# Kernel tuning notes

Hardware: AMD Instinct MI355X
Metric: run time of the kernel (lower is better)

The kernel has to match this reference:

```python
import jax, jax.numpy as jnp
import numpy as np

N_LAYERS = 3
HEADS = 2
HID = 64
IN_DIM = 10
NEG_SLOPE = 0.2  # DGL EGATConv leaky_relu default
B, NPG = 8, 6250  # batch_size, nodes per graph (== max_n_nodes)
N = B * NPG
E = 500000
N_RES = 30  # max_n_resources


def _mlp2(x, W0, b0, W1, b1):
    return jax.nn.relu(x @ W0 + b0) @ W1 + b1


def _segment_softmax(e, dst, n):
    # softmax over incoming edges of each destination node (DGL edge_softmax)
    m = jax.ops.segment_max(e, dst, num_segments=n)
    m = jnp.where(jnp.isfinite(m), m, 0.0)
    ex = jnp.exp(e - m[dst])
    s = jax.ops.segment_sum(ex, dst, num_segments=n)
    return ex / (s[dst] + 1e-9)


def _egat(h, f, src, dst, W_ni, W_nj, W_fij, W_node, attn, bias):
    # per-edge attention features: f_ni[src] + f_nj[dst] + f_fij + bias
    f_out = (h @ W_ni)[src] + (h @ W_nj)[dst] + f @ W_fij + bias   # (E, H*HID)
    f_out = jax.nn.leaky_relu(f_out, NEG_SLOPE).reshape(-1, HEADS, HID)
    e = (f_out * attn[None]).sum(-1)                               # (E, H)
    alpha = _segment_softmax(e, dst, h.shape[0])
    msg = alpha[:, :, None] * (h @ W_node).reshape(-1, HEADS, HID)[src]
    h_out = jax.ops.segment_sum(msg, dst, num_segments=h.shape[0])  # (N, H, HID)
    return h_out, f_out


def _forward(feat, att_rc, att_rp, etype_emb, rid_emb, rc_W, rc_b, rp_W, rp_b,
             fe_W0, fe_b0, fe_W1, fe_b1,
             W_ni, W_nj, W_fij, W_node, attn, egat_bias,
             Wm0, bm0, Wm1, bm1, src, dst, etype, rid):
    feats_list = [feat]
    h = _mlp2(feat, fe_W0, fe_b0, fe_W1, fe_b1)
    feats_list.append(h)
    # 'sum' edge embedding flavor
    emb = etype_emb[etype] + rid_emb[rid] + (att_rc @ rc_W + rc_b) + (att_rp @ rp_W + rp_b)
    for l in range(N_LAYERS):
        h_att, _ = _egat(h, emb, src, dst, W_ni[l], W_nj[l], W_fij[l], W_node[l],
                         attn[l], egat_bias[l])
        h = _mlp2(h_att.reshape(-1, HEADS * HID), Wm0[l], bm0[l], Wm1[l], bm1[l]) + feats_list[-1]
        feats_list.append(h)
    features = jnp.concatenate(feats_list, axis=1)       # (N, IN_DIM + HID*(L+1))
    node_features = features.reshape(B, NPG, -1)
    graph_embedding = node_features.max(axis=1)          # graph_pooling='max'
    rep = jnp.broadcast_to(graph_embedding[:, None, :], node_features.shape)
    return jnp.concatenate([node_features, rep], axis=2)  # (B, NPG, 2*F)


def setup_inputs():
    key = jax.random.key(0)
    ks = iter(jax.random.split(key, 40))
    def rn(shape, s=0.1):
        return jax.random.normal(next(ks), shape, dtype=jnp.float32) * s
    HO = HEADS * HID
    inp = {}
    inp['feat'] = rn((N, IN_DIM), 1.0)
    inp['att_rc'] = rn((E, 2), 1.0)
    inp['att_rp'] = rn((E, 3), 1.0)
    inp['etype_emb'] = rn((7, HID))
    inp['rid_emb'] = rn((N_RES + 1, HID))
    inp['rc_W'] = rn((2, HID)); inp['rc_b'] = rn((HID,))
    inp['rp_W'] = rn((3, HID)); inp['rp_b'] = rn((HID,))
    inp['fe_W0'] = rn((IN_DIM, HID)); inp['fe_b0'] = rn((HID,))
    inp['fe_W1'] = rn((HID, HID)); inp['fe_b1'] = rn((HID,))
    inp['W_ni'] = rn((N_LAYERS, HID, HO)); inp['W_nj'] = rn((N_LAYERS, HID, HO))
    inp['W_fij'] = rn((N_LAYERS, HID, HO)); inp['W_node'] = rn((N_LAYERS, HID, HO))
    inp['attn'] = rn((N_LAYERS, HEADS, HID)); inp['egat_bias'] = rn((N_LAYERS, HO))
    inp['Wm0'] = rn((N_LAYERS, HO, HO)); inp['bm0'] = rn((N_LAYERS, HO))
    inp['Wm1'] = rn((N_LAYERS, HO, HID)); inp['bm1'] = rn((N_LAYERS, HID))
    inp['src'] = jax.random.randint(next(ks), (E,), 0, N, dtype=jnp.int32)
    inp['dst'] = jax.random.randint(next(ks), (E,), 0, N, dtype=jnp.int32)
    inp['etype'] = jax.random.randint(next(ks), (E,), 0, 7, dtype=jnp.int32)
    inp['rid'] = jax.random.randint(next(ks), (E,), 0, N_RES + 1, dtype=jnp.int32)
    return inp


def reference(feat, att_rc, att_rp, etype_emb, rid_emb, rc_W, rc_b, rp_W, rp_b,
              fe_W0, fe_b0, fe_W1, fe_b1, W_ni, W_nj, W_fij, W_node, attn, egat_bias,
              Wm0, bm0, Wm1, bm1, src, dst, etype, rid):
    return _forward(feat, att_rc, att_rp, etype_emb, rid_emb, rc_W, rc_b, rp_W, rp_b,
                    fe_W0, fe_b0, fe_W1, fe_b1, W_ni, W_nj, W_fij, W_node, attn, egat_bias,
                    Wm0, bm0, Wm1, bm1, src, dst, etype, rid)
```

## Files before the change

kernel.cpp:

```cpp
#include <hip/hip_runtime.h>
#include <hip/hip_bf16.h>
#include <math.h>

#define N_NODES 50000
#define N_EDGES 500000
#define B_GRAPHS 8
#define NPG 6250
#define HID 64
#define HO 128
#define IN_DIM 10
#define F_TOT 266
#define OUT_C 532
#define NEG_SLOPE 0.2f
#define NT_ROWS 44
#define SCB 200
#define SCH 250

typedef short bf16x8 __attribute__((ext_vector_type(8)));
typedef float f32x4 __attribute__((ext_vector_type(4)));
typedef float f32x2 __attribute__((ext_vector_type(2)));
typedef unsigned u32x2v __attribute__((ext_vector_type(2)));

__device__ __forceinline__ float LD(const void* p, size_t i, int f32) {
    if (f32) return ((const float*)p)[i];
    unsigned u = ((const unsigned short*)p)[i];
    return __uint_as_float(u << 16);
}
__device__ __forceinline__ unsigned fkey(float f) {
    unsigned b = __float_as_uint(f);
    return (b & 0x80000000u) ? ~b : (b | 0x80000000u);
}
__device__ __forceinline__ float funkey(unsigned k) {
    unsigned b = (k & 0x80000000u) ? (k & 0x7fffffffu) : ~k;
    return __uint_as_float(b);
}
__device__ __forceinline__ unsigned short rnebf(float x) {
    unsigned u = __float_as_uint(x);
    return (unsigned short)((u + 0x7FFFu + ((u >> 16) & 1u)) >> 16);
}
__device__ __forceinline__ unsigned pk2(float lo, float hi) {
    return (unsigned)rnebf(lo) | ((unsigned)rnebf(hi) << 16);
}
__device__ __forceinline__ float plo(unsigned u) { return __uint_as_float(u << 16); }
__device__ __forceinline__ float phi(unsigned u) { return __uint_as_float(u & 0xFFFF0000u); }
__device__ __forceinline__ f32x2 up2(unsigned u) {
    return (f32x2){__uint_as_float(u << 16), __uint_as_float(u & 0xFFFF0000u)};
}
__device__ __forceinline__ void pswap(float& a, float& b) {
    u32x2v r = __builtin_amdgcn_permlane32_swap(__float_as_uint(a), __float_as_uint(b),
                                                false, false);
    a = __uint_as_float(r.x);
    b = __uint_as_float(r.y);
}

__global__ void k_detect(const void* __restrict__ att_rc, int* __restrict__ flagp) {
    __shared__ int cnt;
    if (threadIdx.x == 0) cnt = 0;
    __syncthreads();
    const unsigned short* w = (const unsigned short*)att_rc;
    int c = 0;
    for (int i = threadIdx.x; i < 8192; i += 256) {
        unsigned e = (w[i] >> 7) & 0xFF;
        if (e >= 0xC0) c++;
    }
    atomicAdd(&cnt, c);
    __syncthreads();
    if (threadIdx.x == 0) *flagp = (cnt > 8) ? 1 : 0;
}

__global__ void k_wprep(const void* __restrict__ W_ni, const void* __restrict__ W_nj,
                        const void* __restrict__ W_node, const void* __restrict__ Wm0,
                        const void* __restrict__ Wm1,
                        unsigned short* __restrict__ pw_n,
                        unsigned short* __restrict__ pw_m0,
                        unsigned short* __restrict__ pw_m1,
                        const int* __restrict__ flagp) {
    const int f32 = *flagp;
    int i = blockIdx.x * 256 + threadIdx.x;
    if (i < 73728) {
        int k = i & 63, c = (i >> 6) & 127, lm = i >> 13;
        int m = lm % 3, l = lm / 3;
        const void* W = (m == 0) ? W_ni : (m == 1) ? W_nj : W_node;
        pw_n[i] = rnebf(LD(W, (size_t)l * 8192 + k * 128 + c, f32));
    } else if (i < 73728 + 49152) {
        int j = i - 73728;
        int k = j & 127, c = (j >> 7) & 127, l = j >> 14;
        pw_m0[j] = rnebf(LD(Wm0, (size_t)l * 16384 + k * 128 + c, f32));
    } else if (i < 147456) {
        int j = i - 122880;
        int k = j & 127, c = (j >> 7) & 63, l = j >> 13;
        pw_m1[j] = rnebf(LD(Wm1, (size_t)l * 8192 + k * 64 + c, f32));
    }
}

__global__ void k_count(const int* __restrict__ dst, int* __restrict__ cnt) {
    int i = blockIdx.x * blockDim.x + threadIdx.x;
    int stride = gridDim.x * blockDim.x;
    for (int e = i; e < N_EDGES; e += stride) atomicAdd(&cnt[dst[e]], 1);
}

__global__ void k_scan1(const int* __restrict__ cnt, int* __restrict__ bsum) {
    __shared__ int red[256];
    int b = blockIdx.x, t = threadIdx.x;
    red[t] = (t < SCH) ? cnt[b * SCH + t] : 0;
    __syncthreads();
    for (int off = 128; off; off >>= 1) {
        if (t < off) red[t] += red[t + off];
        __syncthreads();
    }
    if (t == 0) bsum[b] = red[0];
}
__global__ void k_scan2(const int* __restrict__ bsum, int* __restrict__ boff) {
    __shared__ int ts[256];
    int t = threadIdx.x;
    int v = (t < SCB) ? bsum[t] : 0;
    ts[t] = v;
    __syncthreads();
    for (int off = 1; off < 256; off <<= 1) {
        int u = (t >= off) ? ts[t - off] : 0;
        __syncthreads();
        ts[t] += u;
        __syncthreads();
    }
    if (t < SCB) boff[t] = ts[t] - v;
}
__global__ void k_scan3(const int* __restrict__ cnt, const int* __restrict__ boff,
                        int* __restrict__ rowptr, int* __restrict__ cursor) {
    __shared__ int ts[256];
    int b = blockIdx.x, t = threadIdx.x;
    int base = b * SCH;
    int v = (t < SCH) ? cnt[base + t] : 0;
    ts[t] = v;
    __syncthreads();
    for (int off = 1; off < 256; off <<= 1) {
        int u = (t >= off) ? ts[t - off] : 0;
        __syncthreads();
        ts[t] += u;
        __syncthreads();
    }
    if (t < SCH) {
        int r = boff[b] + ts[t] - v;
        rowptr[base + t] = r;
        cursor[base + t] = r;
    }
    if (b == SCB - 1 && t == SCH - 1) rowptr[N_NODES] = boff[b] + ts[t];
}

__global__ void k_fill(const int* __restrict__ src, const int* __restrict__ dst,
                       const int* __restrict__ etype, const int* __restrict__ rid,
                       const void* __restrict__ att_rc, const void* __restrict__ att_rp,
                       int* __restrict__ cursor, uint4* __restrict__ emeta,
                       const int* __restrict__ flagp) {
    const int f32 = *flagp;
    int i = blockIdx.x * blockDim.x + threadIdx.x;
    int stride = gridDim.x * blockDim.x;
    for (int e = i; e < N_EDGES; e += stride) {
        int d = dst[e];
        int j = atomicAdd(&cursor[d], 1);
        float rc0 = LD(att_rc, 2 * (size_t)e, f32), rc1 = LD(att_rc, 2 * (size_t)e + 1, f32);
        float rp0 = LD(att_rp, 3 * (size_t)e, f32), rp1 = LD(att_rp, 3 * (size_t)e + 1, f32),
              rp2 = LD(att_rp, 3 * (size_t)e + 2, f32);
        uint4 m;
        m.x = pk2(rc0, rc1);
        m.y = pk2(rp0, rp1);
        m.z = pk2(rp2, 0.f);
        m.w = (unsigned)(etype[e] | (rid[e] << 3) | ((unsigned)src[e] << 8));
        emeta[j] = m;
    }
}

__global__ void k_init(const void* __restrict__ feat,
                       const void* __restrict__ W0, const void* __restrict__ b0,
                       const void* __restrict__ W1, const void* __restrict__ b1,
                       float* __restrict__ feats, const int* __restrict__ flagp) {
    const int f32 = *flagp;
    __shared__ float sf[64 * 12];
    __shared__ float sW0[IN_DIM * 64];
    __shared__ float sb0[64], sb1[64];
    __shared__ float sh[64 * 64];
    __shared__ float sW1[64 * 64];
    int tid = threadIdx.x, n0 = blockIdx.x * 64;
    for (int i = tid; i < IN_DIM * 64; i += 256) sW0[i] = LD(W0, i, f32);
    for (int i = tid; i < 64; i += 256) { sb0[i] = LD(b0, i, f32); sb1[i] = LD(b1, i, f32); }
    for (int i = tid; i < 64 * 64; i += 256) sW1[i] = LD(W1, i, f32);
    for (int i = tid; i < 64 * IN_DIM; i += 256) {
        int n = n0 + i / IN_DIM, c = i % IN_DIM;
        sf[(i / IN_DIM) * 12 + c] = (n < N_NODES) ? LD(feat, (size_t)n * IN_DIM + c, f32) : 0.f;
    }
    __syncthreads();
    int ng = tid / 16, cg = tid % 16;
    float acc[4][4];
    #pragma unroll
    for (int i = 0; i < 4; i++)
        #pragma unroll
        for (int j = 0; j < 4; j++) acc[i][j] = sb0[cg * 4 + j];
    #pragma unroll
    for (int k = 0; k < IN_DIM; k++)
        #pragma unroll
        for (int i = 0; i < 4; i++) {
            float a = sf[(ng * 4 + i) * 12 + k];
            #pragma unroll
            for (int j = 0; j < 4; j++) acc[i][j] += a * sW0[k * 64 + cg * 4 + j];
        }
    #pragma unroll
    for (int i = 0; i < 4; i++)
        #pragma unroll
        for (int j = 0; j < 4; j++) sh[(ng * 4 + i) * 64 + cg * 4 + j] = fmaxf(acc[i][j], 0.f);
    __syncthreads();
    float o[4][4];
    #pragma unroll
    for (int i = 0; i < 4; i++)
        #pragma unroll
        for (int j = 0; j < 4; j++) o[i][j] = sb1[cg * 4 + j];
    for (int k = 0; k < 64; k++) {
        float4 bv = *(const float4*)&sW1[k * 64 + cg * 4];
        #pragma unroll
        for (int i = 0; i < 4; i++) {
            float a = sh[(ng * 4 + i) * 64 + k];
            o[i][0] += a * bv.x; o[i][1] += a * bv.y;
            o[i][2] += a * bv.z; o[i][3] += a * bv.w;
        }
    }
    #pragma unroll
    for (int i = 0; i < 4; i++) {
        int n = n0 + ng * 4 + i;
        if (n < N_NODES) {
            float* r = feats + (size_t)n * F_TOT;
            #pragma unroll
            for (int j = 0; j < 4; j++) r[IN_DIM + cg * 4 + j] = o[i][j];
        }
    }
    for (int i = tid; i < 64 * IN_DIM; i += 256) {
        int n = n0 + i / IN_DIM, c = i % IN_DIM;
        if (n < N_NODES) feats[(size_t)n * F_TOT + c] = sf[(i / IN_DIM) * 12 + c];
    }
}

__global__ void k_tables(const void* __restrict__ etype_emb, const void* __restrict__ rid_emb,
                         const void* __restrict__ rc_W, const void* __restrict__ rc_b,
                         const void* __restrict__ rp_W, const void* __restrict__ rp_b,
                         const void* __restrict__ W_fij, const void* __restrict__ egat_bias,
                         float* __restrict__ T, const int* __restrict__ flagp) {
    const int f32 = *flagp;
    int l = blockIdx.x;
    __shared__ float S[NT_ROWS * HID];
    __shared__ float W[HID * HO];
    for (int i = threadIdx.x; i < 7 * HID; i += 256) S[i] = LD(etype_emb, i, f32);
    for (int i = threadIdx.x; i < 31 * HID; i += 256) S[7 * HID + i] = LD(rid_emb, i, f32);
    for (int i = threadIdx.x; i < 2 * HID; i += 256) S[38 * HID + i] = LD(rc_W, i, f32);
    for (int i = threadIdx.x; i < 3 * HID; i += 256) S[40 * HID + i] = LD(rp_W, i, f32);
    for (int i = threadIdx.x; i < HID; i += 256)
        S[43 * HID + i] = LD(rc_b, i, f32) + LD(rp_b, i, f32);
    for (int i = threadIdx.x; i < HID * HO; i += 256)
        W[i] = LD(W_fij, (size_t)l * HID * HO + i, f32);
    __syncthreads();
    for (int idx = threadIdx.x; idx < NT_ROWS * HO; idx += 256) {
        int r = idx / HO, c = idx % HO;
        float acc = (r == 43) ? LD(egat_bias, l * HO + c, f32) : 0.f;
        for (int k = 0; k < HID; k++) acc += S[r * HID + k] * W[k * HO + c];
        T[(size_t)l * NT_ROWS * HO + idx] = acc;
    }
}

__global__ void __launch_bounds__(256) k_ngemm(
        const float* __restrict__ feats, int h_off,
        const unsigned short* __restrict__ pw_n, int l,
        unsigned* __restrict__ gsrc, unsigned* __restrict__ gdst) {
    __shared__ __align__(16) unsigned short Xs[64 * 72];
    __shared__ __align__(16) unsigned short Ws[384 * 72];
    int tid = threadIdx.x, n0 = blockIdx.x * 64;
    for (int i = tid; i < 64 * 64; i += 256) {
        int n = i >> 6, c = i & 63, gn = n0 + n;
        Xs[n * 72 + c] = rnebf((gn < N_NODES) ? feats[(size_t)gn * F_TOT + h_off + c] : 0.f);
    }
    const uint4* pn = (const uint4*)pw_n + (size_t)l * 3072;
    for (int i = tid; i < 3072; i += 256) {
        int kq = i & 7, mc = i >> 3;
        *(uint4*)&Ws[mc * 72 + kq * 8] = pn[i];
    }
    __syncthreads();
    int wid = tid >> 6, lane = tid & 63;
    int row0 = wid * 16, mrow = lane & 15, quad = lane >> 4;
    bf16x8 a0 = *(const bf16x8*)&Xs[(row0 + mrow) * 72 + quad * 8];
    bf16x8 a1 = *(const bf16x8*)&Xs[(row0 + mrow) * 72 + 32 + quad * 8];
    f32x4 accA[8], accB[8];
    #pragma unroll
    for (int j = 0; j < 8; j++) { accA[j] = (f32x4){0,0,0,0}; accB[j] = (f32x4){0,0,0,0}; }
    #pragma unroll
    for (int j = 0; j < 8; j++) {
        bf16x8 b0 = *(const bf16x8*)&Ws[(0 * 128 + j * 16 + mrow) * 72 + quad * 8];
        bf16x8 b1 = *(const bf16x8*)&Ws[(0 * 128 + j * 16 + mrow) * 72 + 32 + quad * 8];
        accA[j] = __builtin_amdgcn_mfma_f32_16x16x32_bf16(a0, b0, accA[j], 0, 0, 0);
        accA[j] = __builtin_amdgcn_mfma_f32_16x16x32_bf16(a1, b1, accA[j], 0, 0, 0);
        bf16x8 c0 = *(const bf16x8*)&Ws[(2 * 128 + j * 16 + mrow) * 72 + quad * 8];
        bf16x8 c1 = *(const bf16x8*)&Ws[(2 * 128 + j * 16 + mrow) * 72 + 32 + quad * 8];
        accB[j] = __builtin_amdgcn_mfma_f32_16x16x32_bf16(a0, c0, accB[j], 0, 0, 0);
        accB[j] = __builtin_amdgcn_mfma_f32_16x16x32_bf16(a1, c1, accB[j], 0, 0, 0);
    }
    #pragma unroll
    for (int j = 0; j < 4; j++) {
        int c = j * 16 + mrow;
        #pragma unroll
        for (int r = 0; r < 4; r++) {
            int gn = n0 + row0 + quad * 4 + r;
            if (gn < N_NODES) {
                uint2 v;
                v.x = pk2(accA[j][r], accA[j + 4][r]);
                v.y = pk2(accB[j][r], accB[j + 4][r]);
                *(uint2*)&gsrc[(size_t)gn * 128 + c * 2] = v;
            }
        }
    }
    f32x4 accC[8];
    #pragma unroll
    for (int j = 0; j < 8; j++) accC[j] = (f32x4){0,0,0,0};
    #pragma unroll
    for (int j = 0; j < 8; j++) {
        bf16x8 b0 = *(const bf16x8*)&Ws[(1 * 128 + j * 16 + mrow) * 72 + quad * 8];
        bf16x8 b1 = *(const bf16x8*)&Ws[(1 * 128 + j * 16 + mrow) * 72 + 32 + quad * 8];
        accC[j] = __builtin_amdgcn_mfma_f32_16x16x32_bf16(a0, b0, accC[j], 0, 0, 0);
        accC[j] = __builtin_amdgcn_mfma_f32_16x16x32_bf16(a1, b1, accC[j], 0, 0, 0);
    }
    #pragma unroll
    for (int j = 0; j < 4; j++) {
        int c = j * 16 + mrow;
        #pragma unroll
        for (int r = 0; r < 4; r++) {
            int gn = n0 + row0 + quad * 4 + r;
            if (gn < N_NODES)
                gdst[(size_t)gn * 64 + c] = pk2(accC[j][r], accC[j + 4][r]);
        }
    }
}

__global__ void __launch_bounds__(256) k_edge_fused(
        const float* __restrict__ T, const void* __restrict__ attn, int l,
        const unsigned* __restrict__ gsrc, const unsigned* __restrict__ gdst,
        const int* __restrict__ rowptr, const uint4* __restrict__ emeta,
        float* __restrict__ h_att, const int* __restrict__ flagp) {
    const int f32 = *flagp;
    __shared__ f32x2 Ts2[38 * 64];
    const float* Tl = T + (size_t)l * NT_ROWS * HO;
    int tid = threadIdx.x;
    for (int i = tid; i < 38 * 64; i += 256) {
        int r = i >> 6, c = i & 63;
        Ts2[i] = (f32x2){Tl[r * HO + c], Tl[r * HO + 64 + c]};
    }
    int lane = tid & 63;
    f32x2 C2[6];
    #pragma unroll
    for (int r = 0; r < 6; r++)
        C2[r] = (f32x2){Tl[(38 + r) * HO + lane], Tl[(38 + r) * HO + 64 + lane]};
    const float LOG2E = 1.4426950408889634f;
    f32x2 AT2 = (f32x2){LD(attn, l * HO + lane, f32) * LOG2E,
                        LD(attn, l * HO + 64 + lane, f32) * LOG2E};
    __syncthreads();
    int wid = tid >> 6;
    int d0 = blockIdx.x * 8 + wid * 2;

    #pragma unroll 1
    for (int dn = 0; dn < 2; dn++) {
        int d = d0 + dn;
        int jb = __builtin_amdgcn_readfirstlane(rowptr[d]);
        int je = __builtin_amdgcn_readfirstlane(rowptr[d + 1]);
        int last = je - 1;
        if (last < jb) last = jb;
        if (last > N_EDGES - 1) last = N_EDGES - 1;
        unsigned gd = gdst[(size_t)d * 64 + lane];
        f32x2 NJ2 = up2(gd) + C2[5];
        f32x2 A2 = (f32x2){0.f, 0.f};
        float Lsp = 0.f;

        auto fe = [&](int j_) -> uint4 {
            int jj = (j_ < last) ? j_ : last;
            jj = __builtin_amdgcn_readfirstlane(jj);
            return emeta[jj];
        };
        auto fg = [&](const uint4& em) -> uint2 {
            return *(const uint2*)&gsrc[(size_t)(em.w >> 8) * 128 + lane * 2];
        };
        auto logits = [&](const uint4& em, const uint2& g, float& s_out, f32x2& h2) {
            int et = (int)(em.w & 7u), ri = (int)((em.w >> 3) & 31u);
            f32x2 x = up2(g.x) + NJ2;
            x += Ts2[et * 64 + lane];
            x += Ts2[(7 + ri) * 64 + lane];
            x += plo(em.x) * C2[0];
            x += phi(em.x) * C2[1];
            x += plo(em.y) * C2[2];
            x += phi(em.y) * C2[3];
            x += plo(em.z) * C2[4];
            f32x2 xs = x * NEG_SLOPE;
            x = __builtin_elementwise_max(x, xs);
            f32x2 p = x * AT2;
            h2 = up2(g.y);
            float pa = p.x, pb = p.y;
            pswap(pa, pb);
            float s = pa + pb;
            s += __int_as_float(__builtin_amdgcn_update_dpp(0, __float_as_int(s), 0xB1, 0xF, 0xF, true));
            s += __int_as_float(__builtin_amdgcn_update_dpp(0, __float_as_int(s), 0x4E, 0xF, 0xF, true));
            s += __int_as_float(__builtin_amdgcn_update_dpp(0, __float_as_int(s), 0x141, 0xF, 0xF, true));
            s += __int_as_float(__builtin_amdgcn_update_dpp(0, __float_as_int(s), 0x140, 0xF, 0xF, true));
            s += __int_as_float(__builtin_amdgcn_ds_swizzle(__float_as_int(s), 0x401F));
            s_out = s;
        };
        auto upd = [&](float w, f32x2 h2) {
            Lsp += w;
            float wa = w, wb = w;
            pswap(wa, wb);
            A2 += (f32x2){wa, wb} * h2;
        };

        uint4 eA0 = fe(jb),     eA1 = fe(jb + 1), eA2 = fe(jb + 2), eA3 = fe(jb + 3);
        uint4 eB0 = fe(jb + 4), eB1 = fe(jb + 5), eB2 = fe(jb + 6), eB3 = fe(jb + 7);
        uint2 gA0 = fg(eA0), gA1 = fg(eA1), gA2 = fg(eA2), gA3 = fg(eA3);
        int j = jb;
        #pragma unroll 1
        while (j < je) {
            uint4 eC0 = fe(j + 8), eC1 = fe(j + 9), eC2 = fe(j + 10), eC3 = fe(j + 11);
            uint2 gB0 = fg(eB0), gB1 = fg(eB1), gB2 = fg(eB2), gB3 = fg(eB3);
            {
                float s0, s1, s2, s3;
                f32x2 h0, h1, h2v, h3;
                logits(eA0, gA0, s0, h0);
                logits(eA1, gA1, s1, h1);
                logits(eA2, gA2, s2, h2v);
                logits(eA3, gA3, s3, h3);
                float w0 = __builtin_exp2f(s0);
                float w1 = (j + 1 < je) ? __builtin_exp2f(s1) : 0.f;
                float w2 = (j + 2 < je) ? __builtin_exp2f(s2) : 0.f;
                float w3 = (j + 3 < je) ? __builtin_exp2f(s3) : 0.f;
                upd(w0, h0); upd(w1, h1); upd(w2, h2v); upd(w3, h3);
            }
            if (j + 4 >= je) break;
            uint4 eD0 = fe(j + 12), eD1 = fe(j + 13), eD2 = fe(j + 14), eD3 = fe(j + 15);
            uint2 gN0 = fg(eC0), gN1 = fg(eC1), gN2 = fg(eC2), gN3 = fg(eC3);
            {
                float s0, s1, s2, s3;
                f32x2 h0, h1, h2v, h3;
                logits(eB0, gB0, s0, h0);
                logits(eB1, gB1, s1, h1);
                logits(eB2, gB2, s2, h2v);
                logits(eB3, gB3, s3, h3);
                float w0 = __builtin_exp2f(s0);
                float w1 = (j + 5 < je) ? __builtin_exp2f(s1) : 0.f;
                float w2 = (j + 6 < je) ? __builtin_exp2f(s2) : 0.f;
                float w3 = (j + 7 < je) ? __builtin_exp2f(s3) : 0.f;
                upd(w0, h0); upd(w1, h1); upd(w2, h2v); upd(w3, h3);
            }
            eA0 = eC0; eA1 = eC1; eA2 = eC2; eA3 = eC3;
            eB0 = eD0; eB1 = eD1; eB2 = eD2; eB3 = eD3;
            gA0 = gN0; gA1 = gN1; gA2 = gN2; gA3 = gN3;
            j += 8;
        }

        float la = Lsp, lb = Lsp;
        pswap(la, lb);
        h_att[(size_t)d * HO + lane]      = A2.x / (la + 1e-9f);
        h_att[(size_t)d * HO + 64 + lane] = A2.y / (lb + 1e-9f);
    }
}

__global__ void __launch_bounds__(256) k_mlp(
        const float* __restrict__ h_att,
        const unsigned short* __restrict__ pw_m0, const void* __restrict__ bm0,
        const unsigned short* __restrict__ pw_m1, const void* __restrict__ bm1, int l,
        float* __restrict__ feats, int prev_off, int out_off,
        const int* __restrict__ flagp) {
    const int f32 = *flagp;
    __shared__ __align__(16) unsigned short Xs[64 * 136];
    __shared__ __align__(16) unsigned short W0T[128 * 136];
    __shared__ __align__(16) unsigned short W1T[64 * 136];
    __shared__ float sb0[HO], sb1[64];
    int tid = threadIdx.x, n0 = blockIdx.x * 64;
    for (int i = tid; i < 64 * 128; i += 256) {
        int n = i >> 7, c = i & 127, gn = n0 + n;
        Xs[n * 136 + c] = rnebf((gn < N_NODES) ? h_att[(size_t)gn * HO + c] : 0.f);
    }
    const uint4* p0 = (const uint4*)pw_m0 + (size_t)l * 2048;
    for (int i = tid; i < 2048; i += 256) {
        int kq = i & 15, c = i >> 4;
        *(uint4*)&W0T[c * 136 + kq * 8] = p0[i];
    }
    const uint4* p1 = (const uint4*)pw_m1 + (size_t)l * 1024;
    for (int i = tid; i < 1024; i += 256) {
        int kq = i & 15, c = i >> 4;
        *(uint4*)&W1T[c * 136 + kq * 8] = p1[i];
    }
    for (int i = tid; i < HO; i += 256) sb0[i] = LD(bm0, l * HO + i, f32);
    for (int i = tid; i < 64; i += 256) sb1[i] = LD(bm1, l * 64 + i, f32);
    __syncthreads();
    int wid = tid >> 6, lane = tid & 63;
    int row0 = wid * 16, mrow = lane & 15, quad = lane >> 4;
    f32x4 acc[8];
    #pragma unroll
    for (int j = 0; j < 8; j++) {
        float b = sb0[j * 16 + mrow];
        acc[j] = (f32x4){b, b, b, b};
    }
    #pragma unroll
    for (int ks = 0; ks < 4; ks++) {
        bf16x8 a = *(const bf16x8*)&Xs[(row0 + mrow) * 136 + ks * 32 + quad * 8];
        #pragma unroll
        for (int j = 0; j < 8; j++) {
            bf16x8 b = *(const bf16x8*)&W0T[(j * 16 + mrow) * 136 + ks * 32 + quad * 8];
            acc[j] = __builtin_amdgcn_mfma_f32_16x16x32_bf16(a, b, acc[j], 0, 0, 0);
        }
    }
    #pragma unroll
    for (int j = 0; j < 8; j++)
        #pragma unroll
        for (int r = 0; r < 4; r++)
            Xs[(row0 + quad * 4 + r) * 136 + j * 16 + mrow] = rnebf(fmaxf(acc[j][r], 0.f));
    f32x4 o[4];
    #pragma unroll
    for (int j = 0; j < 4; j++) {
        float b = sb1[j * 16 + mrow];
        o[j] = (f32x4){b, b, b, b};
    }
    #pragma unroll
    for (int ks = 0; ks < 4; ks++) {
        bf16x8 a = *(const bf16x8*)&Xs[(row0 + mrow) * 136 + ks * 32 + quad * 8];
        #pragma unroll
        for (int j = 0; j < 4; j++) {
            bf16x8 b = *(const bf16x8*)&W1T[(j * 16 + mrow) * 136 + ks * 32 + quad * 8];
            o[j] = __builtin_amdgcn_mfma_f32_16x16x32_bf16(a, b, o[j], 0, 0, 0);
        }
    }
    #pragma unroll
    for (int j = 0; j < 4; j++) {
        int c = j * 16 + mrow;
        #pragma unroll
        for (int r = 0; r < 4; r++) {
            int gn = n0 + row0 + quad * 4 + r;
            if (gn < N_NODES) {
                float* rw = feats + (size_t)gn * F_TOT;
                rw[out_off + c] = o[j][r] + rw[prev_off + c];
            }
        }
    }
}

__global__ void k_pool(const float* __restrict__ feats, unsigned* __restrict__ gmax) {
    int g = blockIdx.x;
    int chunk = blockIdx.y;
    int t = threadIdx.x;
    const int CS = 49;
    int nb = chunk * CS;
    int ne = (nb + CS < NPG) ? nb + CS : NPG;
    float m0 = -INFINITY, m1 = -INFINITY;
    for (int n = nb; n < ne; n++) {
        const float* row = feats + (size_t)(g * NPG + n) * F_TOT;
        m0 = fmaxf(m0, row[t]);
        if (t + 256 < F_TOT) m1 = fmaxf(m1, row[t + 256]);
    }
    atomicMax(&gmax[g * F_TOT + t], fkey(m0));
    if (t + 256 < F_TOT) atomicMax(&gmax[g * F_TOT + t + 256], fkey(m1));
}

__global__ void k_out(const float* __restrict__ feats, const unsigned* __restrict__ gmax,
                      void* __restrict__ out, const int* __restrict__ flagp) {
    const int f32 = *flagp;
    int lane = threadIdx.x & 63;
    int wave = (blockIdx.x * blockDim.x + threadIdx.x) >> 6;
    int nw = (gridDim.x * blockDim.x) >> 6;
    for (int row = wave; row < B_GRAPHS * NPG; row += nw) {
        int g = row / NPG;
        const float* fr = feats + (size_t)row * F_TOT;
        const unsigned* gr = gmax + g * F_TOT;
        if (f32) {
            float* o = (float*)out + (size_t)row * OUT_C;
            for (int c = lane; c < OUT_C; c += 64)
                o[c] = (c < F_TOT) ? fr[c] : funkey(gr[c - F_TOT]);
        } else {
            __hip_bfloat16* o = (__hip_bfloat16*)out + (size_t)row * OUT_C;
            for (int c = lane; c < OUT_C; c += 64)
                o[c] = __float2bfloat16((c < F_TOT) ? fr[c] : funkey(gr[c - F_TOT]));
        }
    }
}

extern "C" void kernel_launch(void* const* d_in, const int* in_sizes, int n_in,
                              void* d_out, int out_size, void* d_ws, size_t ws_size,
                              hipStream_t stream) {
    const void* feat      = d_in[0];
    const void* att_rc    = d_in[1];
    const void* att_rp    = d_in[2];
    const void* etype_emb = d_in[3];
    const void* rid_emb   = d_in[4];
    const void* rc_W      = d_in[5];
    const void* rc_b      = d_in[6];
    const void* rp_W      = d_in[7];
    const void* rp_b      = d_in[8];
    const void* fe_W0     = d_in[9];
    const void* fe_b0     = d_in[10];
    const void* fe_W1     = d_in[11];
    const void* fe_b1     = d_in[12];
    const void* W_ni      = d_in[13];
    const void* W_nj      = d_in[14];
    const void* W_fij     = d_in[15];
    const void* W_node    = d_in[16];
    const void* attn      = d_in[17];
    const void* egat_bias = d_in[18];
    const void* Wm0       = d_in[19];
    const void* bm0       = d_in[20];
    const void* Wm1       = d_in[21];
    const void* bm1       = d_in[22];
    const int* src   = (const int*)d_in[23];
    const int* dst   = (const int*)d_in[24];
    const int* etype = (const int*)d_in[25];
    const int* rid   = (const int*)d_in[26];

    char* p = (char*)d_ws;
    auto alloc = [&](size_t bytes) {
        char* r = p;
        p += (bytes + 255) & ~(size_t)255;
        return r;
    };
    float*    feats  = (float*)alloc((size_t)N_NODES * F_TOT * 4);
    unsigned* gsrc   = (unsigned*)alloc((size_t)N_NODES * HO * 4);
    unsigned* gdst   = (unsigned*)alloc((size_t)N_NODES * 64 * 4);
    float*    h_att  = (float*)alloc((size_t)N_NODES * HO * 4);
    float*    T      = (float*)alloc((size_t)3 * NT_ROWS * HO * 4);
    unsigned* gmax   = (unsigned*)alloc((size_t)B_GRAPHS * F_TOT * 4);
    int*      flagp  = (int*)alloc(256);
    int*      rowptr = (int*)alloc((size_t)(N_NODES + 1) * 4);
    int*      cursor = (int*)alloc((size_t)N_NODES * 4);
    int*      cnt    = (int*)alloc((size_t)N_NODES * 4);
    int*      bsum   = (int*)alloc((size_t)SCB * 4);
    int*      boff   = (int*)alloc((size_t)SCB * 4);
    uint4*    emeta  = (uint4*)alloc((size_t)N_EDGES * 16);
    unsigned short* pw_n  = (unsigned short*)alloc((size_t)73728 * 2);
    unsigned short* pw_m0 = (unsigned short*)alloc((size_t)49152 * 2);
    unsigned short* pw_m1 = (unsigned short*)alloc((size_t)24576 * 2);

    k_detect<<<1, 256, 0, stream>>>(att_rc, flagp);
    hipMemsetAsync(cnt, 0, (size_t)N_NODES * 4, stream);
    hipMemsetAsync(gmax, 0, (size_t)B_GRAPHS * F_TOT * 4, stream);
    k_wprep<<<576, 256, 0, stream>>>(W_ni, W_nj, W_node, Wm0, Wm1,
                                     pw_n, pw_m0, pw_m1, flagp);
    k_count<<<512, 256, 0, stream>>>(dst, cnt);
    k_scan1<<<SCB, 256, 0, stream>>>(cnt, bsum);
    k_scan2<<<1, 256, 0, stream>>>(bsum, boff);
    k_scan3<<<SCB, 256, 0, stream>>>(cnt, boff, rowptr, cursor);
    k_fill<<<1024, 256, 0, stream>>>(src, dst, etype, rid, att_rc, att_rp,
                                     cursor, emeta, flagp);
    k_init<<<(N_NODES + 63) / 64, 256, 0, stream>>>(feat, fe_W0, fe_b0, fe_W1, fe_b1,
                                                    feats, flagp);
    k_tables<<<3, 256, 0, stream>>>(etype_emb, rid_emb, rc_W, rc_b, rp_W, rp_b,
                                    W_fij, egat_bias, T, flagp);
    for (int l = 0; l < 3; l++) {
        int h_off = IN_DIM + l * HID;
        int out_off = IN_DIM + (l + 1) * HID;
        k_ngemm<<<(N_NODES + 63) / 64, 256, 0, stream>>>(feats, h_off, pw_n, l, gsrc, gdst);
        k_edge_fused<<<N_NODES / 8, 256, 0, stream>>>(T, attn, l, gsrc, gdst,
                                                      rowptr, emeta, h_att, flagp);
        k_mlp<<<(N_NODES + 63) / 64, 256, 0, stream>>>(h_att, pw_m0, bm0, pw_m1, bm1, l,
                                                       feats, h_off, out_off, flagp);
    }
    k_pool<<<dim3(B_GRAPHS, 128), 256, 0, stream>>>(feats, gmax);
    k_out<<<2048, 256, 0, stream>>>(feats, gmax, d_out, flagp);
}
```

Measured before the change: 720.1 us.

## Fuse next-layer node GEMM into MLP kernel and merge setup kernels

The node projection GEMM for the next layer is folded into the MLP kernel's epilogue. The freshly computed h stays in shared memory as bf16 and feeds MFMA directly, so k_ngemm does not have to reload it from feats. Setup work is also consolidated: the memsets and k_tables go into k_wprep as extra blocks, and scan2 is merged into scan3 by having each block reduce its own prefix of the block sums. This removes several launches and a global round-trip of h, at the cost of a larger shared-memory footprint in k_mlp (about 72 KB), which can lower occupancy.

```diff
diff --git a/kernel.cpp b/kernel.cpp
--- a/kernel.cpp
+++ b/kernel.cpp
@@ -74,22 +74,59 @@
                         unsigned short* __restrict__ pw_n,
                         unsigned short* __restrict__ pw_m0,
                         unsigned short* __restrict__ pw_m1,
-                        const int* __restrict__ flagp) {
+                        const int* __restrict__ flagp,
+                        const void* __restrict__ etype_emb, const void* __restrict__ rid_emb,
+                        const void* __restrict__ rc_W, const void* __restrict__ rc_b,
+                        const void* __restrict__ rp_W, const void* __restrict__ rp_b,
+                        const void* __restrict__ W_fij, const void* __restrict__ egat_bias,
+                        float* __restrict__ T,
+                        int* __restrict__ cnt, unsigned* __restrict__ gmax) {
+    __shared__ float S[NT_ROWS * HID];
+    __shared__ float W[HID * HO];
     const int f32 = *flagp;
-    int i = blockIdx.x * 256 + threadIdx.x;
-    if (i < 73728) {
-        int k = i & 63, c = (i >> 6) & 127, lm = i >> 13;
-        int m = lm % 3, l = lm / 3;
-        const void* W = (m == 0) ? W_ni : (m == 1) ? W_nj : W_node;
-        pw_n[i] = rnebf(LD(W, (size_t)l * 8192 + k * 128 + c, f32));
-    } else if (i < 73728 + 49152) {
-        int j = i - 73728;
-        int k = j & 127, c = (j >> 7) & 127, l = j >> 14;
-        pw_m0[j] = rnebf(LD(Wm0, (size_t)l * 16384 + k * 128 + c, f32));
-    } else if (i < 147456) {
-        int j = i - 122880;
-        int k = j & 127, c = (j >> 7) & 63, l = j >> 13;
-        pw_m1[j] = rnebf(LD(Wm1, (size_t)l * 8192 + k * 64 + c, f32));
+    int b = blockIdx.x;
+    if (b < 576) {
+        int i = b * 256 + threadIdx.x;
+        if (i < 73728) {
+            int k = i & 63, c = (i >> 6) & 127, lm = i >> 13;
+            int m = lm % 3, l = lm / 3;
+            const void* Wp = (m == 0) ? W_ni : (m == 1) ? W_nj : W_node;
+            pw_n[i] = rnebf(LD(Wp, (size_t)l * 8192 + k * 128 + c, f32));
+        } else if (i < 73728 + 49152) {
+            int j = i - 73728;
+            int k = j & 127, c = (j >> 7) & 127, l = j >> 14;
+            pw_m0[j] = rnebf(LD(Wm0, (size_t)l * 16384 + k * 128 + c, f32));
+        } else if (i < 147456) {
+            int j = i - 122880;
+            int k = j & 127, c = (j >> 7) & 63, l = j >> 13;
+            pw_m1[j] = rnebf(LD(Wm1, (size_t)l * 8192 + k * 64 + c, f32));
+        }
+    } else if (b < 780) {
+        int i2 = (b - 576) * 256 + threadIdx.x;
+        if (i2 < N_NODES) cnt[i2] = 0;
+        else {
+            int g = i2 - N_NODES;
+            if (g < B_GRAPHS * F_TOT) gmax[g] = 0;
+        }
+    } else {
+        int l = b - 780;
+        if (l < 3) {
+            for (int i = threadIdx.x; i < 7 * HID; i += 256) S[i] = LD(etype_emb, i, f32);
+            for (int i = threadIdx.x; i < 31 * HID; i += 256) S[7 * HID + i] = LD(rid_emb, i, f32);
+            for (int i = threadIdx.x; i < 2 * HID; i += 256) S[38 * HID + i] = LD(rc_W, i, f32);
+            for (int i = threadIdx.x; i < 3 * HID; i += 256) S[40 * HID + i] = LD(rp_W, i, f32);
+            for (int i = threadIdx.x; i < HID; i += 256)
+                S[43 * HID + i] = LD(rc_b, i, f32) + LD(rp_b, i, f32);
+            for (int i = threadIdx.x; i < HID * HO; i += 256)
+                W[i] = LD(W_fij, (size_t)l * HID * HO + i, f32);
+            __syncthreads();
+            for (int idx = threadIdx.x; idx < NT_ROWS * HO; idx += 256) {
+                int r = idx / HO, c = idx % HO;
+                float acc = (r == 43) ? LD(egat_bias, l * HO + c, f32) : 0.f;
+                for (int k = 0; k < HID; k++) acc += S[r * HID + k] * W[k * HO + c];
+                T[(size_t)l * NT_ROWS * HO + idx] = acc;
+            }
+        }
     }
 }
 
@@ -110,10 +147,21 @@
     }
     if (t == 0) bsum[b] = red[0];
 }
-__global__ void k_scan2(const int* __restrict__ bsum, int* __restrict__ boff) {
+__global__ void k_scan3(const int* __restrict__ cnt, const int* __restrict__ bsum,
+                        int* __restrict__ rowptr, int* __restrict__ cursor) {
+    __shared__ int red[256];
     __shared__ int ts[256];
-    int t = threadIdx.x;
-    int v = (t < SCB) ? bsum[t] : 0;
+    int b = blockIdx.x, t = threadIdx.x;
+    red[t] = (t < b && t < SCB) ? bsum[t] : 0;
+    __syncthreads();
+    for (int off = 128; off; off >>= 1) {
+        if (t < off) red[t] += red[t + off];
+        __syncthreads();
+    }
+    int boff_b = red[0];
+    __syncthreads();
+    int base = b * SCH;
+    int v = (t < SCH) ? cnt[base + t] : 0;
     ts[t] = v;
     __syncthreads();
     for (int off = 1; off < 256; off <<= 1) {
@@ -122,28 +170,12 @@
         ts[t] += u;
         __syncthreads();
     }
-    if (t < SCB) boff[t] = ts[t] - v;
-}
-__global__ void k_scan3(const int* __restrict__ cnt, const int* __restrict__ boff,
-                        int* __restrict__ rowptr, int* __restrict__ cursor) {
-    __shared__ int ts[256];
-    int b = blockIdx.x, t = threadIdx.x;
-    int base = b * SCH;
-    int v = (t < SCH) ? cnt[base + t] : 0;
-    ts[t] = v;
-    __syncthreads();
-    for (int off = 1; off < 256; off <<= 1) {
-        int u = (t >= off) ? ts[t - off] : 0;
-        __syncthreads();
-        ts[t] += u;
-        __syncthreads();
-    }
     if (t < SCH) {
-        int r = boff[b] + ts[t] - v;
+        int r = boff_b + ts[t] - v;
         rowptr[base + t] = r;
         cursor[base + t] = r;
     }
-    if (b == SCB - 1 && t == SCH - 1) rowptr[N_NODES] = boff[b] + ts[t];
+    if (b == SCB - 1 && t == SCH - 1) rowptr[N_NODES] = boff_b + ts[t];
 }
 
 __global__ void k_fill(const int* __restrict__ src, const int* __restrict__ dst,
@@ -233,32 +265,6 @@
     for (int i = tid; i < 64 * IN_DIM; i += 256) {
         int n = n0 + i / IN_DIM, c = i % IN_DIM;
         if (n < N_NODES) feats[(size_t)n * F_TOT + c] = sf[(i / IN_DIM) * 12 + c];
-    }
-}
-
-__global__ void k_tables(const void* __restrict__ etype_emb, const void* __restrict__ rid_emb,
-                         const void* __restrict__ rc_W, const void* __restrict__ rc_b,
-                         const void* __restrict__ rp_W, const void* __restrict__ rp_b,
-                         const void* __restrict__ W_fij, const void* __restrict__ egat_bias,
-                         float* __restrict__ T, const int* __restrict__ flagp) {
-    const int f32 = *flagp;
-    int l = blockIdx.x;
-    __shared__ float S[NT_ROWS * HID];
-    __shared__ float W[HID * HO];
-    for (int i = threadIdx.x; i < 7 * HID; i += 256) S[i] = LD(etype_emb, i, f32);
-    for (int i = threadIdx.x; i < 31 * HID; i += 256) S[7 * HID + i] = LD(rid_emb, i, f32);
-    for (int i = threadIdx.x; i < 2 * HID; i += 256) S[38 * HID + i] = LD(rc_W, i, f32);
-    for (int i = threadIdx.x; i < 3 * HID; i += 256) S[40 * HID + i] = LD(rp_W, i, f32);
-    for (int i = threadIdx.x; i < HID; i += 256)
-        S[43 * HID + i] = LD(rc_b, i, f32) + LD(rp_b, i, f32);
-    for (int i = threadIdx.x; i < HID * HO; i += 256)
-        W[i] = LD(W_fij, (size_t)l * HID * HO + i, f32);
-    __syncthreads();
-    for (int idx = threadIdx.x; idx < NT_ROWS * HO; idx += 256) {
-        int r = idx / HO, c = idx % HO;
-        float acc = (r == 43) ? LD(egat_bias, l * HO + c, f32) : 0.f;
-        for (int k = 0; k < HID; k++) acc += S[r * HID + k] * W[k * HO + c];
-        T[(size_t)l * NT_ROWS * HO + idx] = acc;
     }
 }
 
@@ -465,12 +471,17 @@
         const unsigned short* __restrict__ pw_m0, const void* __restrict__ bm0,
         const unsigned short* __restrict__ pw_m1, const void* __restrict__ bm1, int l,
         float* __restrict__ feats, int prev_off, int out_off,
-        const int* __restrict__ flagp) {
+        const int* __restrict__ flagp,
+        const unsigned short* __restrict__ pw_n, int l_next,
+        unsigned* __restrict__ gsrc, unsigned* __restrict__ gdst, int do_ng) {
     const int f32 = *flagp;
-    __shared__ __align__(16) unsigned short Xs[64 * 136];
-    __shared__ __align__(16) unsigned short W0T[128 * 136];
-    __shared__ __align__(16) unsigned short W1T[64 * 136];
-    __shared__ float sb0[HO], sb1[64];
+    __shared__ __align__(16) char SM[73472];
+    unsigned short* Xs  = (unsigned short*)SM;
+    unsigned short* W0T = (unsigned short*)(SM + 17408);
+    unsigned short* W1T = (unsigned short*)(SM + 52224);
+    unsigned short* WsN = (unsigned short*)(SM + 17408);
+    float* sb0 = (float*)(SM + 72704);
+    float* sb1 = (float*)(SM + 73216);
     int tid = threadIdx.x, n0 = blockIdx.x * 64;
     for (int i = tid; i < 64 * 128; i += 256) {
         int n = i >> 7, c = i & 127, gn = n0 + n;
@@ -532,9 +543,76 @@
         #pragma unroll
         for (int r = 0; r < 4; r++) {
             int gn = n0 + row0 + quad * 4 + r;
+            float outv = 0.f;
             if (gn < N_NODES) {
                 float* rw = feats + (size_t)gn * F_TOT;
-                rw[out_off + c] = o[j][r] + rw[prev_off + c];
+                outv = o[j][r] + rw[prev_off + c];
+                rw[out_off + c] = outv;
+            }
+            o[j][r] = outv;
+        }
+    }
+    if (do_ng) {
+        #pragma unroll
+        for (int j = 0; j < 4; j++)
+            #pragma unroll
+            for (int r = 0; r < 4; r++)
+                Xs[(row0 + quad * 4 + r) * 136 + j * 16 + mrow] = rnebf(o[j][r]);
+        __syncthreads();
+        const uint4* pn = (const uint4*)pw_n + (size_t)l_next * 3072;
+        for (int i = tid; i < 3072; i += 256) {
+            int kq = i & 7, mc = i >> 3;
+            *(uint4*)&WsN[mc * 72 + kq * 8] = pn[i];
+        }
+        __syncthreads();
+        bf16x8 a0 = *(const bf16x8*)&Xs[(row0 + mrow) * 136 + quad * 8];
+        bf16x8 a1 = *(const bf16x8*)&Xs[(row0 + mrow) * 136 + 32 + quad * 8];
+        f32x4 accA[8], accB[8];
+        #pragma unroll
+        for (int j = 0; j < 8; j++) { accA[j] = (f32x4){0,0,0,0}; accB[j] = (f32x4){0,0,0,0}; }
+        #pragma unroll
+        for (int j = 0; j < 8; j++) {
+            bf16x8 b0 = *(const bf16x8*)&WsN[(0 * 128 + j * 16 + mrow) * 72 + quad * 8];
+            bf16x8 b1 = *(const bf16x8*)&WsN[(0 * 128 + j * 16 + mrow) * 72 + 32 + quad * 8];
+            accA[j] = __builtin_amdgcn_mfma_f32_16x16x32_bf16(a0, b0, accA[j], 0, 0, 0);
+            accA[j] = __builtin_amdgcn_mfma_f32_16x16x32_bf16(a1, b1, accA[j], 0, 0, 0);
+            bf16x8 c0 = *(const bf16x8*)&WsN[(2 * 128 + j * 16 + mrow) * 72 + quad * 8];
+            bf16x8 c1 = *(const bf16x8*)&WsN[(2 * 128 + j * 16 + mrow) * 72 + 32 + quad * 8];
+            accB[j] = __builtin_amdgcn_mfma_f32_16x16x32_bf16(a0, c0, accB[j], 0, 0, 0);
+            accB[j] = __builtin_amdgcn_mfma_f32_16x16x32_bf16(a1, c1, accB[j], 0, 0, 0);
+        }
+        #pragma unroll
+        for (int j = 0; j < 4; j++) {
+            int c = j * 16 + mrow;
+            #pragma unroll
+            for (int r = 0; r < 4; r++) {
+                int gn = n0 + row0 + quad * 4 + r;
+                if (gn < N_NODES) {
+                    uint2 v;
+                    v.x = pk2(accA[j][r], accA[j + 4][r]);
+                    v.y = pk2(accB[j][r], accB[j + 4][r]);
+                    *(uint2*)&gsrc[(size_t)gn * 128 + c * 2] = v;
+                }
+            }
+        }
+        f32x4 accC[8];
+        #pragma unroll
+        for (int j = 0; j < 8; j++) accC[j] = (f32x4){0,0,0,0};
+        #pragma unroll
+        for (int j = 0; j < 8; j++) {
+            bf16x8 b0 = *(const bf16x8*)&WsN[(1 * 128 + j * 16 + mrow) * 72 + quad * 8];
+            bf16x8 b1 = *(const bf16x8*)&WsN[(1 * 128 + j * 16 + mrow) * 72 + 32 + quad * 8];
+            accC[j] = __builtin_amdgcn_mfma_f32_16x16x32_bf16(a0, b0, accC[j], 0, 0, 0);
+            accC[j] = __builtin_amdgcn_mfma_f32_16x16x32_bf16(a1, b1, accC[j], 0, 0, 0);
+        }
+        #pragma unroll
+        for (int j = 0; j < 4; j++) {
+            int c = j * 16 + mrow;
+            #pragma unroll
+            for (int r = 0; r < 4; r++) {
+                int gn = n0 + row0 + quad * 4 + r;
+                if (gn < N_NODES)
+                    gdst[(size_t)gn * 64 + c] = pk2(accC[j][r], accC[j + 4][r]);
             }
         }
     }
@@ -627,35 +705,33 @@
     int*      cursor = (int*)alloc((size_t)N_NODES * 4);
     int*      cnt    = (int*)alloc((size_t)N_NODES * 4);
     int*      bsum   = (int*)alloc((size_t)SCB * 4);
-    int*      boff   = (int*)alloc((size_t)SCB * 4);
     uint4*    emeta  = (uint4*)alloc((size_t)N_EDGES * 16);
     unsigned short* pw_n  = (unsigned short*)alloc((size_t)73728 * 2);
     unsigned short* pw_m0 = (unsigned short*)alloc((size_t)49152 * 2);
     unsigned short* pw_m1 = (unsigned short*)alloc((size_t)24576 * 2);
 
     k_detect<<<1, 256, 0, stream>>>(att_rc, flagp);
-    hipMemsetAsync(cnt, 0, (size_t)N_NODES * 4, stream);
-    hipMemsetAsync(gmax, 0, (size_t)B_GRAPHS * F_TOT * 4, stream);
-    k_wprep<<<576, 256, 0, stream>>>(W_ni, W_nj, W_node, Wm0, Wm1,
-                                     pw_n, pw_m0, pw_m1, flagp);
+    k_wprep<<<783, 256, 0, stream>>>(W_ni, W_nj, W_node, Wm0, Wm1,
+                                     pw_n, pw_m0, pw_m1, flagp,
+                                     etype_emb, rid_emb, rc_W, rc_b, rp_W, rp_b,
+                                     W_fij, egat_bias, T, cnt, gmax);
     k_count<<<512, 256, 0, stream>>>(dst, cnt);
     k_scan1<<<SCB, 256, 0, stream>>>(cnt, bsum);
-    k_scan2<<<1, 256, 0, stream>>>(bsum, boff);
-    k_scan3<<<SCB, 256, 0, stream>>>(cnt, boff, rowptr, cursor);
+    k_scan3<<<SCB, 256, 0, stream>>>(cnt, bsum, rowptr, cursor);
     k_fill<<<1024, 256, 0, stream>>>(src, dst, etype, rid, att_rc, att_rp,
                                      cursor, emeta, flagp);
     k_init<<<(N_NODES + 63) / 64, 256, 0, stream>>>(feat, fe_W0, fe_b0, fe_W1, fe_b1,
                                                     feats, flagp);
-    k_tables<<<3, 256, 0, stream>>>(etype_emb, rid_emb, rc_W, rc_b, rp_W, rp_b,
-                                    W_fij, egat_bias, T, flagp);
+    k_ngemm<<<(N_NODES + 63) / 64, 256, 0, stream>>>(feats, IN_DIM, pw_n, 0, gsrc, gdst);
     for (int l = 0; l < 3; l++) {
         int h_off = IN_DIM + l * HID;
         int out_off = IN_DIM + (l + 1) * HID;
-        k_ngemm<<<(N_NODES + 63) / 64, 256, 0, stream>>>(feats, h_off, pw_n, l, gsrc, gdst);
         k_edge_fused<<<N_NODES / 8, 256, 0, stream>>>(T, attn, l, gsrc, gdst,
                                                       rowptr, emeta, h_att, flagp);
         k_mlp<<<(N_NODES + 63) / 64, 256, 0, stream>>>(h_att, pw_m0, bm0, pw_m1, bm1, l,
-                                                       feats, h_off, out_off, flagp);
+                                                       feats, h_off, out_off, flagp,
+                                                       pw_n, l + 1, gsrc, gdst,
+                                                       (l < 2) ? 1 : 0);
     }
     k_pool<<<dim3(B_GRAPHS, 128), 256, 0, stream>>>(feats, gmax);
     k_out<<<2048, 256, 0, stream>>>(feats, gmax, d_out, flagp);
```

Measured after the change: 677.3 us. 5.9% less time.
